# Kernel tuning notes

Hardware: AMD Instinct MI355X
Metric: run time of the kernel (lower is better)

Reference implementation:

```python
import jax, jax.numpy as jnp
import numpy as np

NUM_EXPERTS = 16
TOP_K = 8
INIT_STD = 0.02

def setup_inputs() -> dict:
    key = jax.random.key(0)
    ks = jax.random.split(key, 5)
    B, S, H, I, E = 2, 2048, 2048, 768, NUM_EXPERTS
    return {
        "hidden_states": jax.random.normal(ks[0], (B, S, H), jnp.float32),
        "w_router": jax.random.normal(ks[1], (H, E), jnp.float32) * INIT_STD,
        "w_gate": jax.random.normal(ks[2], (E, H, I), jnp.float32) * INIT_STD,
        "w_up": jax.random.normal(ks[3], (E, H, I), jnp.float32) * INIT_STD,
        "w_down": jax.random.normal(ks[4], (E, I, H), jnp.float32) * INIT_STD,
    }

def reference(hidden_states, w_router, w_gate, w_up, w_down):
    # Router: logits -> fp32 softmax -> top-k -> renormalize (norm_topk_prob=True)
    router_logits = jnp.einsum("bsh,he->bse", hidden_states, w_router)  # [B,S,E]
    routing_weights = jax.nn.softmax(router_logits.astype(jnp.float32), axis=-1)
    topk_w, topk_idx = jax.lax.top_k(routing_weights, k=TOP_K)  # [B,S,K]
    topk_w = topk_w / topk_w.sum(axis=-1, keepdims=True)
    # Dense per-expert combine weights [B,S,E] (sum over top-k slots matching each expert)
    dense_w = jnp.sum(jax.nn.one_hot(topk_idx, NUM_EXPERTS, dtype=topk_w.dtype) * topk_w[..., None], axis=2)
    dense_w = dense_w.astype(hidden_states.dtype)
    # Every expert runs on all tokens (as in the source loop), vectorized over E
    gate = jax.nn.silu(jnp.einsum("bsh,ehi->besi", hidden_states, w_gate))  # [B,E,S,I]
    up = jnp.einsum("bsh,ehi->besi", hidden_states, w_up)
    expert_out = jnp.einsum("besi,eih->besh", gate * up, w_down)  # [B,E,S,H]
    final = jnp.einsum("bse,besh->bsh", dense_w, expert_out)
    return final, router_logits
```

## Files before the change

kernel.cpp:

```cpp
#include <hip/hip_runtime.h>
#include <hip/hip_bf16.h>


typedef __attribute__((ext_vector_type(8))) short short8;
typedef __attribute__((ext_vector_type(4))) float f32x4;

#define NUM_T 4096
#define DH    2048
#define DI    768
#define NE    16
#define DKD   (NE*DI)
#define HSC_CAP 2560
#define TOK_HALF 2048
#define GU_NT (DH/32)
#define FINAL_ELEMS ((size_t)NUM_T*DH)


static __device__ __forceinline__ unsigned short f2bf(float f) {
  unsigned int u = __builtin_bit_cast(unsigned int, f);
  u += 0x7fffu + ((u >> 16) & 1u);
  return (unsigned short)(u >> 16);
}

static __device__ __forceinline__ float bf2f(unsigned short b) {
  unsigned int u = ((unsigned int)b) << 16;
  return __builtin_bit_cast(float, u);
}

static __device__ __forceinline__ void gload16(const void* g, void* l) {
  __builtin_amdgcn_global_load_lds(
      (__attribute__((address_space(1))) void*)(g),
      (__attribute__((address_space(3))) void*)(l), 16, 0, 0);
}


__global__ __launch_bounds__(256)
void cvt_hidden_k(const float* __restrict__ in, unsigned short* __restrict__ out) {
  size_t i = (size_t)blockIdx.x * 256 + threadIdx.x;
  const float4* p = (const float4*)in + i * 2;
  float4 a = p[0], b = p[1];
  short8 v;
  v[0] = (short)f2bf(a.x); v[1] = (short)f2bf(a.y);
  v[2] = (short)f2bf(a.z); v[3] = (short)f2bf(a.w);
  v[4] = (short)f2bf(b.x); v[5] = (short)f2bf(b.y);
  v[6] = (short)f2bf(b.z); v[7] = (short)f2bf(b.w);
  *(short8*)(out + i * 8) = v;
}


__global__ __launch_bounds__(256)
void transpose_cvt_k(const float* __restrict__ in, unsigned short* __restrict__ out,
                     int C, long inStrideE, long outStrideE, int outLD,
                     int rShift, int rStrd, int rOff) {
  __shared__ float tile[32][33];
  const float* inE = in + (size_t)blockIdx.z * inStrideE;
  unsigned short* outE = out + (size_t)blockIdx.z * outStrideE;
  int c0 = blockIdx.x * 32, r0 = blockIdx.y * 32;
  int tx = threadIdx.x, ty = threadIdx.y;
#pragma unroll
  for (int i = 0; i < 4; i++)
    tile[ty * 4 + i][tx] = inE[(size_t)(r0 + ty * 4 + i) * C + c0 + tx];
  __syncthreads();
#pragma unroll
  for (int i = 0; i < 4; i++) {
    int c = ty * 4 + i;
    int r = c0 + c;
    int s = ((r >> rShift) * rStrd) + rOff + (r & ((1 << rShift) - 1));
    outE[(size_t)s * outLD + r0 + tx] = f2bf(tile[tx][c]);
  }
}


__global__ __launch_bounds__(256)
void router_k(const float* __restrict__ x, const float* __restrict__ wr,
              float* __restrict__ logits_out, unsigned short* __restrict__ dwb,
              unsigned char* __restrict__ slt) {
  int t = blockIdx.x;
  int tid = threadIdx.x, lane = tid & 63, wid = tid >> 6;
  float acc[16];
#pragma unroll
  for (int e = 0; e < 16; e++) acc[e] = 0.f;
  const float* xt = x + (size_t)t * DH;
  for (int i = tid; i < DH; i += 256) {
    float hv = xt[i];
    const float4* w4 = (const float4*)(wr + (size_t)i * 16);
#pragma unroll
    for (int q = 0; q < 4; q++) {
      float4 w = w4[q];
      acc[q * 4 + 0] += hv * w.x; acc[q * 4 + 1] += hv * w.y;
      acc[q * 4 + 2] += hv * w.z; acc[q * 4 + 3] += hv * w.w;
    }
  }
#pragma unroll
  for (int e = 0; e < 16; e++) {
#pragma unroll
    for (int off = 32; off; off >>= 1) acc[e] += __shfl_xor(acc[e], off, 64);
  }
  __shared__ float red[4][16];
  if (lane == 0) {
#pragma unroll
    for (int e = 0; e < 16; e++) red[wid][e] = acc[e];
  }
  __syncthreads();
  if (tid == 0) {
    float lg[16];
#pragma unroll
    for (int e = 0; e < 16; e++) lg[e] = red[0][e] + red[1][e] + red[2][e] + red[3][e];
    float mx = lg[0];
#pragma unroll
    for (int e = 1; e < 16; e++) mx = fmaxf(mx, lg[e]);
    float p[16], s = 0.f;
#pragma unroll
    for (int e = 0; e < 16; e++) { p[e] = __expf(lg[e] - mx); s += p[e]; }
    float inv = 1.f / s;
#pragma unroll
    for (int e = 0; e < 16; e++) p[e] *= inv;
    float tmp[16];
#pragma unroll
    for (int e = 0; e < 16; e++) tmp[e] = p[e];
    int idx[8]; float val[8]; float ts = 0.f;
#pragma unroll
    for (int k = 0; k < 8; k++) {
      int b = 0; float bv = tmp[0];
#pragma unroll
      for (int e = 1; e < 16; e++) { if (tmp[e] > bv) { bv = tmp[e]; b = e; } }
      idx[k] = b; val[k] = bv; tmp[b] = -1.f; ts += bv;
    }
    float dw[16];
    unsigned char sl[16];
#pragma unroll
    for (int e = 0; e < 16; e++) { dw[e] = 0.f; sl[e] = 0xFF; }
    float invt = 1.f / ts;
#pragma unroll
    for (int k = 0; k < 8; k++) { dw[idx[k]] += val[k] * invt; sl[idx[k]] = (unsigned char)k; }
#pragma unroll
    for (int e = 0; e < 16; e++) {
      dwb[(size_t)t * 16 + e] = f2bf(dw[e]);
      slt[(size_t)t * 16 + e] = sl[e];
      logits_out[(size_t)t * 16 + e] = lg[e];
    }
  }
}


__global__ __launch_bounds__(256)
void build_lists_k(const unsigned short* __restrict__ dwb,
                   const unsigned char* __restrict__ slt,
                   unsigned short* __restrict__ lst, int* __restrict__ meta) {
  int e = blockIdx.x;
  int tid = threadIdx.x;
  unsigned short loc[16]; int c = 0;
#pragma unroll
  for (int j = 0; j < 16; j++) {
    int t = tid * 16 + j;
    if (dwb[(size_t)t * 16 + e] != 0) {
      unsigned short s = slt[(size_t)t * 16 + e];
      loc[c++] = (unsigned short)(t | (s << 12));
    }
  }
  __shared__ int sc[256];
  __shared__ int pre[257];
  sc[tid] = c;
  __syncthreads();
  if (tid == 0) {
    int s = 0;
    for (int i = 0; i < 256; i++) { pre[i] = s; s += sc[i]; }
    pre[256] = s;
  }
  __syncthreads();
  unsigned short* L = lst + (size_t)e * NUM_T;
  int base = pre[tid];
  for (int j = 0; j < c; j++) L[base + j] = loc[j];
  int total = pre[256];
  for (int i = total + tid; i < NUM_T; i += 256) L[i] = 0xFFFFu;
  if (tid == 0) { meta[e * 2] = pre[128]; meta[e * 2 + 1] = total; }
}


__global__ __launch_bounds__(256, 2)
void gateup_k(const unsigned short* __restrict__ hbf,
              const unsigned short* __restrict__ wgubt,
              const unsigned short* __restrict__ dwb,
              const unsigned short* __restrict__ lst,
              unsigned short* __restrict__ hsC) {
  const int bxr = blockIdx.x;
  const int wl  = (bxr & 7) * 240 + (bxr >> 3);
  const int e   = wl / 120;
  const int rem = wl - e * 120;
  const int j   = rem / 10;
  const int m0  = (rem % 10) * 256;

  const unsigned short* L = lst + (size_t)e * NUM_T;
  if (L[m0] & 0x8000) return;

  const int tid = threadIdx.x, lane = tid & 63, wid = tid >> 6;
  const int wr = wid >> 1, wc = wid & 1;
  const int lr = lane & 15, lgp = lane >> 4;

  __shared__ alignas(16) unsigned short ALDS[3 * 256 * 32];
  __shared__ alignas(16) unsigned short BLDS[2 * 128 * 32];

  f32x4 zero = {0.f, 0.f, 0.f, 0.f};
  f32x4 acc[8][4];
#pragma unroll
  for (int m = 0; m < 8; m++)
#pragma unroll
    for (int n = 0; n < 4; n++) acc[m][n] = zero;

  const unsigned short* wgubtE = wgubt + (size_t)e * 1536 * DH;

  const int srow    = lane >> 2;
  const int schunk8 = (((lane & 3) - ((lane >> 3) & 3)) & 3) * 8;
  const int slot8   = (((lane >> 4) + ((lane >> 1) & 3)) & 3) * 8;

  const unsigned short* gA[4];
#pragma unroll
  for (int i = 0; i < 4; i++) {
    unsigned short en = L[m0 + wid * 64 + i * 16 + srow];
    size_t tok = (en & 0x8000) ? 0 : (size_t)(en & 0xFFF);
    gA[i] = hbf + tok * DH + schunk8;
  }
  const unsigned short* gB[2];
#pragma unroll
  for (int i = 0; i < 2; i++)
    gB[i] = wgubtE + ((size_t)j * 128 + wid * 32 + i * 16 + srow) * DH + schunk8;

#define STAGE_A(buf, t, i) gload16(gA[i] + (size_t)(t) * 32, \
    ALDS + (buf) * 8192 + (wid * 64 + (i) * 16) * 32)
#define STAGE_B(buf, t, i) gload16(gB[i] + (size_t)(t) * 32, \
    BLDS + (buf) * 4096 + (wid * 32 + (i) * 16) * 32)
#define RD_A(mf) (*(const short8*)(Ab + (wr * 128 + (mf) * 16 + lr) * 32 + slot8))
#define RD_B(nf) (*(const short8*)(Bb + (wc * 64 + (nf) * 16 + lr) * 32 + slot8))
#define MFMA4(m0_, m1_, m2_, m3_, n_) \
    acc[m0_][n_] = __builtin_amdgcn_mfma_f32_16x16x32_bf16(a[m0_], b[n_], acc[m0_][n_], 0, 0, 0); \
    acc[m1_][n_] = __builtin_amdgcn_mfma_f32_16x16x32_bf16(a[m1_], b[n_], acc[m1_][n_], 0, 0, 0); \
    acc[m2_][n_] = __builtin_amdgcn_mfma_f32_16x16x32_bf16(a[m2_], b[n_], acc[m2_][n_], 0, 0, 0); \
    acc[m3_][n_] = __builtin_amdgcn_mfma_f32_16x16x32_bf16(a[m3_], b[n_], acc[m3_][n_], 0, 0, 0);

  STAGE_B(0, 0, 0); STAGE_B(0, 0, 1);
  STAGE_A(0, 0, 0); STAGE_A(0, 0, 1); STAGE_A(0, 0, 2); STAGE_A(0, 0, 3);
  STAGE_A(1, 1, 0); STAGE_A(1, 1, 1); STAGE_A(1, 1, 2); STAGE_A(1, 1, 3);

  int ra = 0, rb = 0, sa = 2;
  short8 a[8], b[4];
#pragma unroll 1
  for (int t = 0; t < GU_NT; ++t) {
    if (t < GU_NT - 1) asm volatile("s_waitcnt vmcnt(4)" ::: "memory");
    else               asm volatile("s_waitcnt vmcnt(0)" ::: "memory");
    __builtin_amdgcn_s_barrier();
    __builtin_amdgcn_sched_barrier(0);
    const unsigned short* Ab = ALDS + ra * 8192;
    const unsigned short* Bb = BLDS + rb * 4096;
    if (t + 1 < GU_NT) { STAGE_B(rb ^ 1, t + 1, 0); STAGE_B(rb ^ 1, t + 1, 1); }
    a[0] = RD_A(0); a[1] = RD_A(1); a[2] = RD_A(2); a[3] = RD_A(3);
    b[0] = RD_B(0); b[1] = RD_B(1);
    asm volatile("s_waitcnt lgkmcnt(0)" ::: "memory");
    __builtin_amdgcn_sched_barrier(0);
    __builtin_amdgcn_s_setprio(1);
    MFMA4(0, 1, 2, 3, 0); MFMA4(0, 1, 2, 3, 1);
    __builtin_amdgcn_s_setprio(0);
    if (t + 2 < GU_NT) { STAGE_A(sa, t + 2, 0); STAGE_A(sa, t + 2, 1); }
    a[4] = RD_A(4); a[5] = RD_A(5); a[6] = RD_A(6); a[7] = RD_A(7);
    asm volatile("s_waitcnt lgkmcnt(0)" ::: "memory");
    __builtin_amdgcn_sched_barrier(0);
    __builtin_amdgcn_s_setprio(1);
    MFMA4(4, 5, 6, 7, 0); MFMA4(4, 5, 6, 7, 1);
    __builtin_amdgcn_s_setprio(0);
    if (t + 2 < GU_NT) { STAGE_A(sa, t + 2, 2); STAGE_A(sa, t + 2, 3); }
    b[2] = RD_B(2); b[3] = RD_B(3);
    asm volatile("s_waitcnt lgkmcnt(0)" ::: "memory");
    __builtin_amdgcn_sched_barrier(0);
    __builtin_amdgcn_s_setprio(1);
    MFMA4(4, 5, 6, 7, 2); MFMA4(4, 5, 6, 7, 3);
    __builtin_amdgcn_s_setprio(0);
    __builtin_amdgcn_s_setprio(1);
    MFMA4(0, 1, 2, 3, 2); MFMA4(0, 1, 2, 3, 3);
    __builtin_amdgcn_s_setprio(0);
    ra = (ra == 2) ? 0 : ra + 1;
    sa = (sa == 2) ? 0 : sa + 1;
    rb ^= 1;
  }
#undef STAGE_A
#undef STAGE_B
#undef RD_A
#undef RD_B
#undef MFMA4

  __syncthreads();
  unsigned short (*exch)[64] = (unsigned short(*)[64])ALDS;
  if (wc == 1) {
#pragma unroll
    for (int mf = 0; mf < 8; mf++)
#pragma unroll
      for (int nf = 0; nf < 4; nf++)
#pragma unroll
        for (int r = 0; r < 4; r++)
          exch[wr * 128 + mf * 16 + lgp * 4 + r][nf * 16 + lr] = f2bf(acc[mf][nf][r]);
  }
  __syncthreads();
  if (wc == 0) {
#pragma unroll
    for (int mf = 0; mf < 8; mf++) {
#pragma unroll
      for (int r = 0; r < 4; r++) {
        int m = wr * 128 + mf * 16 + lgp * 4 + r;
        unsigned short en = L[m0 + m];
        if (en & 0x8000) continue;
        int tp = en & 0xFFF;
        float w = bf2f(dwb[(size_t)tp * 16 + e]);
#pragma unroll
        for (int nf = 0; nf < 4; nf++) {
          float g = acc[mf][nf][r];
          float u = bf2f(exch[m][nf * 16 + lr]);
          float sig = 1.f / (1.f + __expf(-g));
          hsC[((size_t)e * HSC_CAP + m0 + m) * DI + j * 64 + nf * 16 + lr]
              = f2bf(sig * g * u * w);
        }
      }
    }
  }
}


__global__ __launch_bounds__(256, 3)
void down_half_k(const unsigned short* __restrict__ hsC,
                 const unsigned short* __restrict__ wdbt,
                 const unsigned short* __restrict__ lst,
                 const int* __restrict__ meta,
                 unsigned short* __restrict__ slotbuf, int hf) {
  const int bxr = blockIdx.x;
  const int wl  = (bxr & 7) * 320 + (bxr >> 3);
  const int e   = wl / 160;
  const int rem = wl - e * 160;
  const int n0  = (rem / 10) * 128;
  const int m0  = (rem % 10) * 128;

  const int rs = hf ? meta[e * 2] : 0;
  const int re = hf ? meta[e * 2 + 1] : meta[e * 2];
  const int rcount = re - rs;
  if (m0 >= rcount) return;

  const int tid = threadIdx.x, lane = tid & 63, wid = tid >> 6;
  const int wm = wid >> 1, wn = wid & 1;
  const int lr = lane & 15, lgp = lane >> 4;

  __shared__ alignas(16) unsigned short As[3 * 128 * 32];
  __shared__ alignas(16) unsigned short Bs[3 * 128 * 32];

  f32x4 zero = {0.f, 0.f, 0.f, 0.f};
  f32x4 acc[4][4];
#pragma unroll
  for (int m = 0; m < 4; m++)
#pragma unroll
    for (int n = 0; n < 4; n++) acc[m][n] = zero;

  const int srow    = lane >> 2;
  const int schunk8 = (((lane & 3) - ((lane >> 3) & 3)) & 3) * 8;
  const int sOff0   = wid * 1024;
  const int sOff1   = sOff0 + 512;
  const size_t arow0 = (size_t)(e * HSC_CAP + rs + m0 + wid * 32 + srow);
  const size_t arow1 = arow0 + 16;
  const size_t brow0 = (size_t)(n0 + wid * 32 + srow), brow1 = brow0 + 16;
  const int slot8 = (((lane >> 4) + ((lane >> 1) & 3)) & 3) * 8;

  const unsigned short* wdE = wdbt + (size_t)e * DI;

  auto stage = [&](int b, int k0) {
    unsigned short* Ab = As + b * 4096;
    unsigned short* Bb = Bs + b * 4096;
    gload16(hsC + arow0 * DI + k0 + schunk8, Ab + sOff0);
    gload16(hsC + arow1 * DI + k0 + schunk8, Ab + sOff1);
    gload16(wdE + brow0 * DKD + k0 + schunk8, Bb + sOff0);
    gload16(wdE + brow1 * DKD + k0 + schunk8, Bb + sOff1);
  };

  auto compute = [&](int bsel) {
    const unsigned short* Ab = As + bsel * 4096;
    const unsigned short* Bb = Bs + bsel * 4096;
    short8 a[4], b[4];
#pragma unroll
    for (int m = 0; m < 4; m++)
      a[m] = *(const short8*)(Ab + (size_t)(wm * 64 + m * 16 + lr) * 32 + slot8);
#pragma unroll
    for (int n = 0; n < 4; n++)
      b[n] = *(const short8*)(Bb + (size_t)(wn * 64 + n * 16 + lr) * 32 + slot8);
#pragma unroll
    for (int m = 0; m < 4; m++)
#pragma unroll
      for (int n = 0; n < 4; n++)
        acc[m][n] = __builtin_amdgcn_mfma_f32_16x16x32_bf16(a[m], b[n], acc[m][n], 0, 0, 0);
  };

  const int NT = DI / 32;
  stage(0, 0);
  stage(1, 32);
  int bc = 0, bs = 2;
#pragma unroll 1
  for (int i = 0; i < NT - 1; ++i) {
    asm volatile("s_waitcnt vmcnt(4)" ::: "memory");
    __builtin_amdgcn_s_barrier();
    __builtin_amdgcn_sched_barrier(0);
    compute(bc);
    if (i + 2 < NT) stage(bs, (i + 2) * 32);
    bc = (bc == 2) ? 0 : bc + 1;
    bs = (bs == 2) ? 0 : bs + 1;
  }
  asm volatile("s_waitcnt vmcnt(0)" ::: "memory");
  __builtin_amdgcn_s_barrier();
  __builtin_amdgcn_sched_barrier(0);
  compute(bc);

  const unsigned short* L = lst + (size_t)e * NUM_T;
#pragma unroll
  for (int m = 0; m < 4; m++) {
#pragma unroll
    for (int r = 0; r < 4; r++) {
      int gr = m0 + wm * 64 + m * 16 + 4 * lgp + r;
      if (gr >= rcount) continue;
      unsigned short en = L[rs + gr];
      int t  = en & 0xFFF;
      int s  = (en >> 12) & 7;
      int tl = t - hf * TOK_HALF;
#pragma unroll
      for (int n = 0; n < 4; n++)
        slotbuf[((size_t)s * TOK_HALF + tl) * DH + n0 + wn * 64 + n * 16 + lr] =
            f2bf(acc[m][n][r]);
    }
  }
}


__global__ __launch_bounds__(256)
void reduce_half_k(const unsigned short* __restrict__ slotbuf,
                   float* __restrict__ outp, int hf) {
  size_t i  = (size_t)blockIdx.x * 256 + threadIdx.x;
  size_t tl = i >> 8;
  size_t h0 = (i & 255) * 8;
  float sum[8];
#pragma unroll
  for (int j = 0; j < 8; j++) sum[j] = 0.f;
#pragma unroll
  for (int s = 0; s < 8; s++) {
    short8 v = *(const short8*)(slotbuf + ((size_t)s * TOK_HALF + tl) * DH + h0);
#pragma unroll
    for (int j = 0; j < 8; j++) sum[j] += bf2f((unsigned short)v[j]);
  }
  float* o = outp + ((size_t)(hf * TOK_HALF) + tl) * DH + h0;
  float4 o0 = {sum[0], sum[1], sum[2], sum[3]};
  float4 o1 = {sum[4], sum[5], sum[6], sum[7]};
  *(float4*)o = o0;
  *(float4*)(o + 4) = o1;
}


extern "C" void kernel_launch(void* const* d_in, const int* in_sizes, int n_in,
                              void* d_out, int out_size, void* d_ws, size_t ws_size,
                              hipStream_t stream) {
  const float* x  = (const float*)d_in[0];
  const float* wr = (const float*)d_in[1];
  const float* wg = (const float*)d_in[2];
  const float* wu = (const float*)d_in[3];
  const float* wd = (const float*)d_in[4];

  float* outF = (float*)d_out;
  float* outL = outF + FINAL_ELEMS;

  if (ws_size < 180682880ull) return;
  char* ws = (char*)d_ws;
  unsigned short* hbf   = (unsigned short*)(ws);
  unsigned short* wgubt = (unsigned short*)(ws + 16777216);
  unsigned short* hsC   = (unsigned short*)(ws + 117440512);
  unsigned short* dwb   = (unsigned short*)(ws + 180355072);
  unsigned short* lst   = (unsigned short*)(ws + 180486144);
  unsigned char*  slt   = (unsigned char*) (ws + 180617216);
  int*            meta  = (int*)           (ws + 180682752);
  unsigned short* sbuf  = (unsigned short*)(ws);
  unsigned short* wdbt  = (unsigned short*)(ws + 67108864);

  cvt_hidden_k<<<4096, 256, 0, stream>>>(x, hbf);
  transpose_cvt_k<<<dim3(24, 64, 16), dim3(32, 8), 0, stream>>>(
      wg, wgubt, 768, (long)2048 * 768, (long)1536 * 2048, 2048, 6, 128, 0);
  transpose_cvt_k<<<dim3(24, 64, 16), dim3(32, 8), 0, stream>>>(
      wu, wgubt, 768, (long)2048 * 768, (long)1536 * 2048, 2048, 6, 128, 64);
  router_k<<<4096, 256, 0, stream>>>(x, wr, outL, dwb, slt);
  build_lists_k<<<16, 256, 0, stream>>>(dwb, slt, lst, meta);
  gateup_k<<<1920, 256, 0, stream>>>(hbf, wgubt, dwb, lst, hsC);
  transpose_cvt_k<<<dim3(64, 24, 16), dim3(32, 8), 0, stream>>>(
      wd, wdbt, 2048, (long)768 * 2048, 768L, 12288, 11, 2048, 0);
  down_half_k<<<2560, 256, 0, stream>>>(hsC, wdbt, lst, meta, sbuf, 0);
  reduce_half_k<<<2048, 256, 0, stream>>>(sbuf, outF, 0);
  down_half_k<<<2560, 256, 0, stream>>>(hsC, wdbt, lst, meta, sbuf, 1);
  reduce_half_k<<<2048, 256, 0, stream>>>(sbuf, outF, 1);
}
```

Before: 721.5 us.

## Split gate/up GEMM tile across eight waves with triple-buffered B

The gate/up kernel moves from 256 threads (4 waves, each owning a 128x64 output tile) to 512 threads (8 waves, each owning 64x64), which halves per-wave accumulators. The B operand gets a third LDS buffer so A and B share one three-stage pipeline, and a mid-iteration barrier is added before refilling B. The exchange buffer for the up half gets a padded stride of 68 to avoid LDS bank conflicts. The aim is more latency hiding from extra waves and lower register pressure, at the cost of more barriers, more LDS use and more per-tile instruction overhead. One change to down_half_k is only a cosmetic rewrite of the B read address.

Measured after the change: 655.4 us. 9.2% less time.

```diff
diff --git a/kernel.cpp b/kernel.cpp
--- a/kernel.cpp
+++ b/kernel.cpp
@@ -177,7 +177,7 @@
 }
 
 
-__global__ __launch_bounds__(256, 2)
+__global__ __launch_bounds__(512, 4)
 void gateup_k(const unsigned short* __restrict__ hbf,
               const unsigned short* __restrict__ wgubt,
               const unsigned short* __restrict__ dwb,
@@ -194,16 +194,16 @@
   if (L[m0] & 0x8000) return;
 
   const int tid = threadIdx.x, lane = tid & 63, wid = tid >> 6;
-  const int wr = wid >> 1, wc = wid & 1;
+  const int wm = wid >> 1, wn = wid & 1;
   const int lr = lane & 15, lgp = lane >> 4;
 
   __shared__ alignas(16) unsigned short ALDS[3 * 256 * 32];
-  __shared__ alignas(16) unsigned short BLDS[2 * 128 * 32];
+  __shared__ alignas(16) unsigned short BLDS[3 * 128 * 32];
 
   f32x4 zero = {0.f, 0.f, 0.f, 0.f};
-  f32x4 acc[8][4];
-#pragma unroll
-  for (int m = 0; m < 8; m++)
+  f32x4 acc[4][4];
+#pragma unroll
+  for (int m = 0; m < 4; m++)
 #pragma unroll
     for (int n = 0; n < 4; n++) acc[m][n] = zero;
 
@@ -213,97 +213,86 @@
   const int schunk8 = (((lane & 3) - ((lane >> 3) & 3)) & 3) * 8;
   const int slot8   = (((lane >> 4) + ((lane >> 1) & 3)) & 3) * 8;
 
-  const unsigned short* gA[4];
-#pragma unroll
-  for (int i = 0; i < 4; i++) {
-    unsigned short en = L[m0 + wid * 64 + i * 16 + srow];
+  const unsigned short* gA[2];
+#pragma unroll
+  for (int i = 0; i < 2; i++) {
+    unsigned short en = L[m0 + i * 128 + wid * 16 + srow];
     size_t tok = (en & 0x8000) ? 0 : (size_t)(en & 0xFFF);
     gA[i] = hbf + tok * DH + schunk8;
   }
-  const unsigned short* gB[2];
-#pragma unroll
-  for (int i = 0; i < 2; i++)
-    gB[i] = wgubtE + ((size_t)j * 128 + wid * 32 + i * 16 + srow) * DH + schunk8;
+  const unsigned short* gB = wgubtE + ((size_t)j * 128 + wid * 16 + srow) * DH + schunk8;
 
 #define STAGE_A(buf, t, i) gload16(gA[i] + (size_t)(t) * 32, \
-    ALDS + (buf) * 8192 + (wid * 64 + (i) * 16) * 32)
-#define STAGE_B(buf, t, i) gload16(gB[i] + (size_t)(t) * 32, \
-    BLDS + (buf) * 4096 + (wid * 32 + (i) * 16) * 32)
-#define RD_A(mf) (*(const short8*)(Ab + (wr * 128 + (mf) * 16 + lr) * 32 + slot8))
-#define RD_B(nf) (*(const short8*)(Bb + (wc * 64 + (nf) * 16 + lr) * 32 + slot8))
-#define MFMA4(m0_, m1_, m2_, m3_, n_) \
-    acc[m0_][n_] = __builtin_amdgcn_mfma_f32_16x16x32_bf16(a[m0_], b[n_], acc[m0_][n_], 0, 0, 0); \
-    acc[m1_][n_] = __builtin_amdgcn_mfma_f32_16x16x32_bf16(a[m1_], b[n_], acc[m1_][n_], 0, 0, 0); \
-    acc[m2_][n_] = __builtin_amdgcn_mfma_f32_16x16x32_bf16(a[m2_], b[n_], acc[m2_][n_], 0, 0, 0); \
-    acc[m3_][n_] = __builtin_amdgcn_mfma_f32_16x16x32_bf16(a[m3_], b[n_], acc[m3_][n_], 0, 0, 0);
-
-  STAGE_B(0, 0, 0); STAGE_B(0, 0, 1);
-  STAGE_A(0, 0, 0); STAGE_A(0, 0, 1); STAGE_A(0, 0, 2); STAGE_A(0, 0, 3);
-  STAGE_A(1, 1, 0); STAGE_A(1, 1, 1); STAGE_A(1, 1, 2); STAGE_A(1, 1, 3);
-
-  int ra = 0, rb = 0, sa = 2;
-  short8 a[8], b[4];
+    ALDS + (buf) * 8192 + (i) * 4096 + wid * 512)
+#define STAGE_B(buf, t) gload16(gB + (size_t)(t) * 32, \
+    BLDS + (buf) * 4096 + wid * 512)
+#define RD_A(mf) (*(const short8*)(Ab + (wm * 64 + (mf) * 16 + lr) * 32 + slot8))
+#define RD_B(nf) (*(const short8*)(Bb + (wn * 64 + (nf) * 16 + lr) * 32 + slot8))
+
+  STAGE_A(0, 0, 0); STAGE_A(0, 0, 1); STAGE_B(0, 0);
+  STAGE_A(1, 1, 0); STAGE_A(1, 1, 1); STAGE_B(1, 1);
+
+  int bc = 0, sb = 2;
+  short8 a[4], b[4];
 #pragma unroll 1
   for (int t = 0; t < GU_NT; ++t) {
-    if (t < GU_NT - 1) asm volatile("s_waitcnt vmcnt(4)" ::: "memory");
+    if (t < GU_NT - 1) asm volatile("s_waitcnt vmcnt(3)" ::: "memory");
     else               asm volatile("s_waitcnt vmcnt(0)" ::: "memory");
     __builtin_amdgcn_s_barrier();
     __builtin_amdgcn_sched_barrier(0);
-    const unsigned short* Ab = ALDS + ra * 8192;
-    const unsigned short* Bb = BLDS + rb * 4096;
-    if (t + 1 < GU_NT) { STAGE_B(rb ^ 1, t + 1, 0); STAGE_B(rb ^ 1, t + 1, 1); }
+    const unsigned short* Ab = ALDS + bc * 8192;
+    const unsigned short* Bb = BLDS + bc * 4096;
+    if (t + 2 < GU_NT) { STAGE_A(sb, t + 2, 0); STAGE_A(sb, t + 2, 1); }
     a[0] = RD_A(0); a[1] = RD_A(1); a[2] = RD_A(2); a[3] = RD_A(3);
     b[0] = RD_B(0); b[1] = RD_B(1);
     asm volatile("s_waitcnt lgkmcnt(0)" ::: "memory");
     __builtin_amdgcn_sched_barrier(0);
     __builtin_amdgcn_s_setprio(1);
-    MFMA4(0, 1, 2, 3, 0); MFMA4(0, 1, 2, 3, 1);
+#pragma unroll
+    for (int m = 0; m < 4; m++) {
+      acc[m][0] = __builtin_amdgcn_mfma_f32_16x16x32_bf16(a[m], b[0], acc[m][0], 0, 0, 0);
+      acc[m][1] = __builtin_amdgcn_mfma_f32_16x16x32_bf16(a[m], b[1], acc[m][1], 0, 0, 0);
+    }
     __builtin_amdgcn_s_setprio(0);
-    if (t + 2 < GU_NT) { STAGE_A(sa, t + 2, 0); STAGE_A(sa, t + 2, 1); }
-    a[4] = RD_A(4); a[5] = RD_A(5); a[6] = RD_A(6); a[7] = RD_A(7);
-    asm volatile("s_waitcnt lgkmcnt(0)" ::: "memory");
-    __builtin_amdgcn_sched_barrier(0);
-    __builtin_amdgcn_s_setprio(1);
-    MFMA4(4, 5, 6, 7, 0); MFMA4(4, 5, 6, 7, 1);
-    __builtin_amdgcn_s_setprio(0);
-    if (t + 2 < GU_NT) { STAGE_A(sa, t + 2, 2); STAGE_A(sa, t + 2, 3); }
+    __builtin_amdgcn_s_barrier();
+    if (t + 2 < GU_NT) STAGE_B(sb, t + 2);
     b[2] = RD_B(2); b[3] = RD_B(3);
     asm volatile("s_waitcnt lgkmcnt(0)" ::: "memory");
     __builtin_amdgcn_sched_barrier(0);
     __builtin_amdgcn_s_setprio(1);
-    MFMA4(4, 5, 6, 7, 2); MFMA4(4, 5, 6, 7, 3);
+#pragma unroll
+    for (int m = 0; m < 4; m++) {
+      acc[m][2] = __builtin_amdgcn_mfma_f32_16x16x32_bf16(a[m], b[2], acc[m][2], 0, 0, 0);
+      acc[m][3] = __builtin_amdgcn_mfma_f32_16x16x32_bf16(a[m], b[3], acc[m][3], 0, 0, 0);
+    }
     __builtin_amdgcn_s_setprio(0);
-    __builtin_amdgcn_s_setprio(1);
-    MFMA4(0, 1, 2, 3, 2); MFMA4(0, 1, 2, 3, 3);
-    __builtin_amdgcn_s_setprio(0);
-    ra = (ra == 2) ? 0 : ra + 1;
-    sa = (sa == 2) ? 0 : sa + 1;
-    rb ^= 1;
+    bc = (bc == 2) ? 0 : bc + 1;
+    sb = (sb == 2) ? 0 : sb + 1;
   }
 #undef STAGE_A
 #undef STAGE_B
 #undef RD_A
 #undef RD_B
-#undef MFMA4
-
-  __syncthreads();
-  unsigned short (*exch)[64] = (unsigned short(*)[64])ALDS;
-  if (wc == 1) {
-#pragma unroll
-    for (int mf = 0; mf < 8; mf++)
+
+  __syncthreads();
+  unsigned short* exch = (unsigned short*)ALDS;
+  if (wn == 1) {
+#pragma unroll
+    for (int mf = 0; mf < 4; mf++)
 #pragma unroll
       for (int nf = 0; nf < 4; nf++)
 #pragma unroll
         for (int r = 0; r < 4; r++)
-          exch[wr * 128 + mf * 16 + lgp * 4 + r][nf * 16 + lr] = f2bf(acc[mf][nf][r]);
-  }
-  __syncthreads();
-  if (wc == 0) {
-#pragma unroll
-    for (int mf = 0; mf < 8; mf++) {
+          exch[(wm * 64 + mf * 16 + lgp * 4 + r) * 68 + nf * 16 + lr]
+              = f2bf(acc[mf][nf][r]);
+  }
+  __syncthreads();
+  if (wn == 0) {
+#pragma unroll
+    for (int mf = 0; mf < 4; mf++) {
 #pragma unroll
       for (int r = 0; r < 4; r++) {
-        int m = wr * 128 + mf * 16 + lgp * 4 + r;
+        int m = wm * 64 + mf * 16 + lgp * 4 + r;
         unsigned short en = L[m0 + m];
         if (en & 0x8000) continue;
         int tp = en & 0xFFF;
@@ -311,7 +300,7 @@
 #pragma unroll
         for (int nf = 0; nf < 4; nf++) {
           float g = acc[mf][nf][r];
-          float u = bf2f(exch[m][nf * 16 + lr]);
+          float u = bf2f(exch[m * 68 + nf * 16 + lr]);
           float sig = 1.f / (1.f + __expf(-g));
           hsC[((size_t)e * HSC_CAP + m0 + m) * DI + j * 64 + nf * 16 + lr]
               = f2bf(sig * g * u * w);
@@ -383,12 +372,13 @@
       a[m] = *(const short8*)(Ab + (size_t)(wm * 64 + m * 16 + lr) * 32 + slot8);
 #pragma unroll
     for (int n = 0; n < 4; n++)
-      b[n] = *(const short8*)(Bb + (size_t)(wn * 64 + n * 16 + lr) * 32 + slot8);
+      b[n] = *(const short8*)(Bs + bsel * 4096 + (size_t)(wn * 64 + n * 16 + lr) * 32 + slot8);
 #pragma unroll
     for (int m = 0; m < 4; m++)
 #pragma unroll
       for (int n = 0; n < 4; n++)
         acc[m][n] = __builtin_amdgcn_mfma_f32_16x16x32_bf16(a[m], b[n], acc[m][n], 0, 0, 0);
+    (void)Bb;
   };
 
   const int NT = DI / 32;
@@ -484,7 +474,7 @@
       wu, wgubt, 768, (long)2048 * 768, (long)1536 * 2048, 2048, 6, 128, 64);
   router_k<<<4096, 256, 0, stream>>>(x, wr, outL, dwb, slt);
   build_lists_k<<<16, 256, 0, stream>>>(dwb, slt, lst, meta);
-  gateup_k<<<1920, 256, 0, stream>>>(hbf, wgubt, dwb, lst, hsC);
+  gateup_k<<<1920, 512, 0, stream>>>(hbf, wgubt, dwb, lst, hsC);
   transpose_cvt_k<<<dim3(64, 24, 16), dim3(32, 8), 0, stream>>>(
       wd, wdbt, 2048, (long)768 * 2048, 768L, 12288, 11, 2048, 0);
   down_half_k<<<2560, 256, 0, stream>>>(hsC, wdbt, lst, meta, sbuf, 0);
```
